# Kernel optimization log

Hardware: AMD Instinct MI355X
Metric: run time of the kernel (lower is better)

## Reference

```python
import jax, jax.numpy as jnp
import numpy as np

VOCAB = 32000
EMB = 300
DEC_UNITS = 512
UNITS = 2 * DEC_UNITS        # GRU units = 1024
ENC_DIM = 1024               # encoder output feature dim
B, S = 256, 128
IN_DIM = ENC_DIM + EMB       # GRU input: [context ; embedding] = 1324


def setup_inputs() -> dict:
    key = jax.random.key(0)
    ks = jax.random.split(key, 16)
    sc = 0.02
    return {
        "x": jax.random.randint(ks[0], (B, 1), 0, VOCAB),
        "state": jax.random.normal(ks[1], (B, UNITS), jnp.float32),
        "encoder_output": jax.random.normal(ks[2], (B, S, ENC_DIM), jnp.float32),
        "emb": jax.random.normal(ks[3], (VOCAB, EMB), jnp.float32) * sc,
        "W1": jax.random.normal(ks[4], (ENC_DIM, DEC_UNITS), jnp.float32) * sc,
        "b1": jnp.zeros((DEC_UNITS,), jnp.float32),
        "W2": jax.random.normal(ks[5], (UNITS, DEC_UNITS), jnp.float32) * sc,
        "b2": jnp.zeros((DEC_UNITS,), jnp.float32),
        "V": jax.random.normal(ks[6], (DEC_UNITS, 1), jnp.float32) * sc,
        "bV": jnp.zeros((1,), jnp.float32),
        "gru_k": jax.random.normal(ks[7], (IN_DIM, 3 * UNITS), jnp.float32) * sc,
        "gru_rk": jax.random.normal(ks[8], (UNITS, 3 * UNITS), jnp.float32) * sc,
        "gru_b": jnp.zeros((2, 3 * UNITS), jnp.float32),  # [input_bias, recurrent_bias] (reset_after=True)
        "fc_W": jax.random.normal(ks[9], (UNITS, VOCAB), jnp.float32) * sc,
        "fc_b": jnp.zeros((VOCAB,), jnp.float32),
    }


def reference(x, state, encoder_output, emb, W1, b1, W2, b2, V, bV,
              gru_k, gru_rk, gru_b, fc_W, fc_b):
    # --- Bahdanau attention (query = state, values = encoder_output) ---
    # score: [B, S, 1]
    q = state @ W2 + b2                                    # [B, U_att]
    score = jnp.tanh(encoder_output @ W1 + b1 + q[:, None, :]) @ V + bV
    attn = jax.nn.softmax(score, axis=1)                   # [B, S, 1]
    context = jnp.sum(attn * encoder_output, axis=1)       # [B, ENC_DIM]

    # --- embed token and concat with context (seq len 1) ---
    x_emb = emb[x[:, 0]]                                   # [B, EMB]
    xi = jnp.concatenate([context, x_emb], axis=-1)        # [B, IN_DIM]

    # --- single GRU step (Keras GRU, reset_after=True, inference: no dropout) ---
    mx = xi @ gru_k + gru_b[0]                             # [B, 3U]
    mh = state @ gru_rk + gru_b[1]                         # [B, 3U]
    xz, xr, xh = jnp.split(mx, 3, axis=-1)
    hz, hr, hh_rec = jnp.split(mh, 3, axis=-1)
    z = jax.nn.sigmoid(xz + hz)
    r = jax.nn.sigmoid(xr + hr)
    hh = jnp.tanh(xh + r * hh_rec)
    h = z * state + (1.0 - z) * hh                         # [B, UNITS]

    # --- softmax projection over vocab ---
    probs = jax.nn.softmax(h @ fc_W + fc_b, axis=-1)       # [B, VOCAB]
    return probs, h, attn
```

## Files before the change

### kernel.cpp

```cpp
#include <hip/hip_runtime.h>
#include <math.h>

#define B_    256
#define S_    128
#define ENCD  1024
#define DECU  512
#define UNITS 1024
#define VOCAB 32000
#define EMB_  300
#define INDIM 1324
#define KPADX 1344
#define G3    3072

typedef __bf16 bf16x8 __attribute__((ext_vector_type(8)));
typedef __bf16 bf16x4 __attribute__((ext_vector_type(4)));
typedef __bf16 bf16x2 __attribute__((ext_vector_type(2)));
typedef float  f32x4  __attribute__((ext_vector_type(4)));

#define MFMA16(a, b, c) __builtin_amdgcn_mfma_f32_16x16x32_bf16((a), (b), (c), 0, 0, 0)

__device__ __forceinline__ int swz(int row, int e) { return row * 64 + (e ^ ((row & 7) << 3)); }

__device__ __forceinline__ void gl_lds16(const void* g, void* l) {
  __builtin_amdgcn_global_load_lds((const __attribute__((address_space(1))) void*)g,
                                   (__attribute__((address_space(3))) void*)l, 16, 0, 0);
}

__device__ __forceinline__ float fast_tanh(float x) {
  x = fminf(fmaxf(x, -15.f), 15.f);
  float e = __expf(2.f * x);
  return (e - 1.f) / (e + 1.f);
}

__global__ __launch_bounds__(256) void k_prep(const float* __restrict__ enc,
                                              __bf16* __restrict__ enc_bf,
                                              const float* __restrict__ state,
                                              __bf16* __restrict__ state_bf) {
  int bid = blockIdx.x;
  if (bid < 4096) {
    for (int g = bid * 256 + threadIdx.x; g < (B_ * S_ * ENCD) / 8; g += 4096 * 256) {
      const float* p = enc + (size_t)g * 8;
      float4 f0 = *(const float4*)p;
      float4 f1 = *(const float4*)(p + 4);
      bf16x8 o = {(__bf16)f0.x, (__bf16)f0.y, (__bf16)f0.z, (__bf16)f0.w,
                  (__bf16)f1.x, (__bf16)f1.y, (__bf16)f1.z, (__bf16)f1.w};
      *(bf16x8*)(enc_bf + (size_t)g * 8) = o;
    }
  } else {
    int i4 = (bid - 4096) * 256 + threadIdx.x;
    float4 f = *(const float4*)(state + (size_t)i4 * 4);
    bf16x4 o = {(__bf16)f.x, (__bf16)f.y, (__bf16)f.z, (__bf16)f.w};
    *(bf16x4*)(state_bf + (size_t)i4 * 4) = o;
  }
}

__global__ __launch_bounds__(1024) void k_w1t(const float* __restrict__ W1,
                                              __bf16* __restrict__ W1t) {
  int n = blockIdx.x;
  int k = threadIdx.x;
  W1t[(size_t)n * 1024 + k] = (__bf16)W1[(size_t)k * 512 + n];
}

template <int BM>
__global__ __launch_bounds__(512) void k_gemm2(const __bf16* __restrict__ A, int ldaK,
                                               const float* __restrict__ B,
                                               const float* __restrict__ bias,
                                               float* __restrict__ C, int K, int N) {
  constexpr int WR = (BM == 64) ? 2 : 4;
  constexpr int WN = 8 / WR;
  constexpr int MI = BM / (WR * 16);
  constexpr int NI = 64 / (WN * 16);
  __shared__ __align__(16) __bf16 As[2][BM * 64];
  __shared__ __align__(16) __bf16 Bs[2][64 * 64];
  int tid = threadIdx.x, lane = tid & 63, w = tid >> 6;
  int wr = w / WN, wn = w % WN;
  int m0 = blockIdx.x * BM, n0 = blockIdx.y * 64;
  int lrow = lane & 15, lk = (lane >> 4) * 8;
  int r0 = wr * MI * 16, c0 = wn * NI * 16;
  f32x4 acc[MI][NI] = {};

  constexpr int ACH = BM / 64;
  constexpr int TPR = 8 / ACH;
  bf16x8 pfa[ACH];
  float pfb[8];
  int am = tid / TPR, aks = (tid % TPR) * (ACH * 8);
  const __bf16* arow = A + (size_t)(m0 + am) * ldaK + aks;
  int bn = tid & 63, bks = (tid >> 6) * 8;
  int nk = (K + 63) >> 6;

#pragma unroll
  for (int c = 0; c < ACH; ++c) pfa[c] = *(const bf16x8*)(arow + c * 8);
#pragma unroll
  for (int i = 0; i < 8; ++i) { int k = bks + i; pfb[i] = (k < K) ? B[(size_t)k * N + n0 + bn] : 0.f; }
#pragma unroll
  for (int c = 0; c < ACH; ++c) *(bf16x8*)&As[0][swz(am, aks + c * 8)] = pfa[c];
  {
    __bf16 tb[8];
#pragma unroll
    for (int i = 0; i < 8; ++i) tb[i] = (__bf16)pfb[i];
    *(bf16x8*)&Bs[0][swz(bn, bks)] = *(bf16x8*)&tb[0];
  }
  __syncthreads();

  int cur = 0;
  for (int it = 0; it < nk; ++it) {
    bool more = (it + 1 < nk);
    if (more) {
      int k0 = (it + 1) * 64;
#pragma unroll
      for (int c = 0; c < ACH; ++c) pfa[c] = *(const bf16x8*)(arow + k0 + c * 8);
#pragma unroll
      for (int i = 0; i < 8; ++i) { int k = k0 + bks + i; pfb[i] = (k < K) ? B[(size_t)k * N + n0 + bn] : 0.f; }
    }
    const __bf16* Ac = As[cur];
    const __bf16* Bc = Bs[cur];
#pragma unroll
    for (int kk = 0; kk < 64; kk += 32) {
      bf16x8 av[MI], bv[NI];
#pragma unroll
      for (int mi = 0; mi < MI; ++mi) { int r = r0 + mi * 16 + lrow; av[mi] = *(const bf16x8*)&Ac[swz(r, kk + lk)]; }
#pragma unroll
      for (int ni = 0; ni < NI; ++ni) { int r = c0 + ni * 16 + lrow; bv[ni] = *(const bf16x8*)&Bc[swz(r, kk + lk)]; }
#pragma unroll
      for (int mi = 0; mi < MI; ++mi)
#pragma unroll
        for (int ni = 0; ni < NI; ++ni) acc[mi][ni] = MFMA16(av[mi], bv[ni], acc[mi][ni]);
    }
    if (more) {
#pragma unroll
      for (int c = 0; c < ACH; ++c) *(bf16x8*)&As[cur ^ 1][swz(am, aks + c * 8)] = pfa[c];
      __bf16 tb[8];
#pragma unroll
      for (int i = 0; i < 8; ++i) tb[i] = (__bf16)pfb[i];
      *(bf16x8*)&Bs[cur ^ 1][swz(bn, bks)] = *(bf16x8*)&tb[0];
      __syncthreads();
      cur ^= 1;
    }
  }
#pragma unroll
  for (int mi = 0; mi < MI; ++mi)
#pragma unroll
    for (int ni = 0; ni < NI; ++ni) {
      int colg = n0 + c0 + ni * 16 + lrow;
      float bvv = bias[colg];
#pragma unroll
      for (int reg = 0; reg < 4; ++reg) {
        int rowg = m0 + r0 + mi * 16 + (lane >> 4) * 4 + reg;
        C[(size_t)rowg * N + colg] = acc[mi][ni][reg] + bvv;
      }
    }
}

__global__ __launch_bounds__(512) void k_gemm2d(const __bf16* __restrict__ A, int ldaK,
                                                const float* __restrict__ B1,
                                                const float* __restrict__ bias1,
                                                float* __restrict__ C1, int N1,
                                                const float* __restrict__ B2,
                                                const float* __restrict__ bias2,
                                                float* __restrict__ C2, int N2,
                                                int K) {
  constexpr int BM = 64, MI = 2, NI = 1;
  __shared__ __align__(16) __bf16 As[2][BM * 64];
  __shared__ __align__(16) __bf16 Bs[2][64 * 64];
  int tid = threadIdx.x, lane = tid & 63, w = tid >> 6;
  int wr = w >> 2, wn = w & 3;
  int m0 = blockIdx.x * BM;
  int n0 = blockIdx.y * 64;
  const float* B; const float* bias; float* C; int N;
  if (n0 < N1) { B = B1; bias = bias1; C = C1; N = N1; }
  else         { B = B2; bias = bias2; C = C2; N = N2; n0 -= N1; }
  int lrow = lane & 15, lk = (lane >> 4) * 8;
  int r0 = wr * MI * 16, c0 = wn * NI * 16;
  f32x4 acc[MI][NI] = {};

  bf16x8 pfa;
  float pfb[8];
  int am = tid >> 3, aks = (tid & 7) * 8;
  const __bf16* arow = A + (size_t)(m0 + am) * ldaK + aks;
  int bn = tid & 63, bks = (tid >> 6) * 8;
  int nk = (K + 63) >> 6;

  pfa = *(const bf16x8*)(arow);
#pragma unroll
  for (int i = 0; i < 8; ++i) { int k = bks + i; pfb[i] = (k < K) ? B[(size_t)k * N + n0 + bn] : 0.f; }
  *(bf16x8*)&As[0][swz(am, aks)] = pfa;
  {
    __bf16 tb[8];
#pragma unroll
    for (int i = 0; i < 8; ++i) tb[i] = (__bf16)pfb[i];
    *(bf16x8*)&Bs[0][swz(bn, bks)] = *(bf16x8*)&tb[0];
  }
  __syncthreads();

  int cur = 0;
  for (int it = 0; it < nk; ++it) {
    bool more = (it + 1 < nk);
    if (more) {
      int k0 = (it + 1) * 64;
      pfa = *(const bf16x8*)(arow + k0);
#pragma unroll
      for (int i = 0; i < 8; ++i) { int k = k0 + bks + i; pfb[i] = (k < K) ? B[(size_t)k * N + n0 + bn] : 0.f; }
    }
    const __bf16* Ac = As[cur];
    const __bf16* Bc = Bs[cur];
#pragma unroll
    for (int kk = 0; kk < 64; kk += 32) {
      bf16x8 av[MI], bv[NI];
#pragma unroll
      for (int mi = 0; mi < MI; ++mi) { int r = r0 + mi * 16 + lrow; av[mi] = *(const bf16x8*)&Ac[swz(r, kk + lk)]; }
#pragma unroll
      for (int ni = 0; ni < NI; ++ni) { int r = c0 + ni * 16 + lrow; bv[ni] = *(const bf16x8*)&Bc[swz(r, kk + lk)]; }
#pragma unroll
      for (int mi = 0; mi < MI; ++mi)
#pragma unroll
        for (int ni = 0; ni < NI; ++ni) acc[mi][ni] = MFMA16(av[mi], bv[ni], acc[mi][ni]);
    }
    if (more) {
      *(bf16x8*)&As[cur ^ 1][swz(am, aks)] = pfa;
      __bf16 tb[8];
#pragma unroll
      for (int i = 0; i < 8; ++i) tb[i] = (__bf16)pfb[i];
      *(bf16x8*)&Bs[cur ^ 1][swz(bn, bks)] = *(bf16x8*)&tb[0];
      __syncthreads();
      cur ^= 1;
    }
  }
#pragma unroll
  for (int mi = 0; mi < MI; ++mi)
#pragma unroll
    for (int ni = 0; ni < NI; ++ni) {
      int colg = n0 + c0 + ni * 16 + lrow;
      float bvv = bias[colg];
#pragma unroll
      for (int reg = 0; reg < 4; ++reg) {
        int rowg = m0 + r0 + mi * 16 + (lane >> 4) * 4 + reg;
        C[(size_t)rowg * N + colg] = acc[mi][ni][reg] + bvv;
      }
    }
}

__global__ __launch_bounds__(512) void k_score8(const __bf16* __restrict__ enc_bf,
                                                const __bf16* __restrict__ W1t,
                                                const float* __restrict__ b1,
                                                const float* __restrict__ q,
                                                const float* __restrict__ V,
                                                float* __restrict__ sc_part) {
  __shared__ __align__(16) __bf16 As[3][128 * 64];
  __shared__ __align__(16) __bf16 Bs[3][128 * 64];
  __shared__ float red[2][128];
  int b = blockIdx.x, by = blockIdx.y;
  int m0 = b * 128, n0 = by * 128;
  int tid = threadIdx.x, lane = tid & 63, w = tid >> 6;
  int wr = w >> 1, wn = w & 1;
  int lrow = lane & 15, lk = (lane >> 4) * 8;
  int r0 = wr * 32, c0 = wn * 64;
  f32x4 acc[2][4] = {};

  float vj[4], b1j[4], qv[4];
#pragma unroll
  for (int ni = 0; ni < 4; ++ni) {
    int j = n0 + c0 + ni * 16 + lrow;
    vj[ni] = V[j]; b1j[ni] = b1[j]; qv[ni] = q[(size_t)b * DECU + j];
  }
  int srow = lane >> 3;
  int sslot = (lane & 7) ^ (srow & 7);
  const __bf16* asrc[2];
  const __bf16* bsrc[2];
  int ch0 = w * 2;
#pragma unroll
  for (int c = 0; c < 2; ++c) {
    int row = (ch0 + c) * 8 + srow;
    asrc[c] = enc_bf + (size_t)(m0 + row) * 1024 + sslot * 8;
    bsrc[c] = W1t + (size_t)(n0 + row) * 1024 + sslot * 8;
  }
  asm volatile("s_waitcnt vmcnt(0)" ::: "memory");

#pragma unroll
  for (int t = 0; t < 2; ++t) {
    int k0 = t * 64;
#pragma unroll
    for (int c = 0; c < 2; ++c) {
      gl_lds16(asrc[c] + k0, &As[t][(ch0 + c) * 512]);
      gl_lds16(bsrc[c] + k0, &Bs[t][(ch0 + c) * 512]);
    }
  }
  asm volatile("s_waitcnt vmcnt(4)" ::: "memory");
  __builtin_amdgcn_s_barrier();

#pragma unroll
  for (int it = 0; it < 16; ++it) {
    if (it + 2 < 16) {
      int k0 = (it + 2) * 64, bi = (it + 2) % 3;
#pragma unroll
      for (int c = 0; c < 2; ++c) {
        gl_lds16(asrc[c] + k0, &As[bi][(ch0 + c) * 512]);
        gl_lds16(bsrc[c] + k0, &Bs[bi][(ch0 + c) * 512]);
      }
    }
    const __bf16* Ac = As[it % 3];
    const __bf16* Bc = Bs[it % 3];
#pragma unroll
    for (int kk = 0; kk < 64; kk += 32) {
      bf16x8 av[2], bv[4];
#pragma unroll
      for (int mi = 0; mi < 2; ++mi) { int r = r0 + mi * 16 + lrow; av[mi] = *(const bf16x8*)&Ac[swz(r, kk + lk)]; }
#pragma unroll
      for (int ni = 0; ni < 4; ++ni) { int r = c0 + ni * 16 + lrow; bv[ni] = *(const bf16x8*)&Bc[swz(r, kk + lk)]; }
#pragma unroll
      for (int mi = 0; mi < 2; ++mi)
#pragma unroll
        for (int ni = 0; ni < 4; ++ni) acc[mi][ni] = MFMA16(av[mi], bv[ni], acc[mi][ni]);
    }
    if (it < 15) {
      if (it < 14) asm volatile("s_waitcnt vmcnt(4)" ::: "memory");
      else         asm volatile("s_waitcnt vmcnt(0)" ::: "memory");
      __builtin_amdgcn_s_barrier();
    }
  }
  float psum[2][4] = {};
#pragma unroll
  for (int mi = 0; mi < 2; ++mi)
#pragma unroll
    for (int ni = 0; ni < 4; ++ni) {
#pragma unroll
      for (int reg = 0; reg < 4; ++reg)
        psum[mi][reg] += vj[ni] * fast_tanh(acc[mi][ni][reg] + b1j[ni] + qv[ni]);
    }
#pragma unroll
  for (int off = 1; off < 16; off <<= 1)
#pragma unroll
    for (int mi = 0; mi < 2; ++mi)
#pragma unroll
      for (int reg = 0; reg < 4; ++reg)
        psum[mi][reg] += __shfl_xor(psum[mi][reg], off);
  __syncthreads();
  if (lrow == 0) {
#pragma unroll
    for (int mi = 0; mi < 2; ++mi)
#pragma unroll
      for (int reg = 0; reg < 4; ++reg)
        red[wn][r0 + mi * 16 + (lane >> 4) * 4 + reg] = psum[mi][reg];
  }
  __syncthreads();
  if (tid < 128)
    sc_part[((size_t)b * 128 + tid) * 4 + by] = red[0][tid] + red[1][tid];
}

__global__ __launch_bounds__(256) void k_ctx4(const float* __restrict__ sc_part,
                                              const float* __restrict__ bV,
                                              const __bf16* __restrict__ enc_bf,
                                              const int* __restrict__ x,
                                              const float* __restrict__ emb,
                                              float* __restrict__ attn_out,
                                              __bf16* __restrict__ xi_bf) {
  int b = blockIdx.x, chunk = blockIdx.y, t = threadIdx.x;
  int lane = t & 63, w = t >> 6;
  __shared__ float a_s[S_];
  __shared__ float part[4][128];
  if (t < S_) {
    float4 p = *(const float4*)&sc_part[((size_t)b * 128 + t) * 4];
    a_s[t] = bV[0] + p.x + p.y + p.z + p.w;
  }
  __syncthreads();
  float mx = -INFINITY;
  for (int s = 0; s < S_; ++s) mx = fmaxf(mx, a_s[s]);
  float sum = 0.f;
  for (int s = 0; s < S_; ++s) sum += __expf(a_s[s] - mx);
  float inv = 1.f / sum;
  __syncthreads();
  if (t < S_) {
    float av = __expf(a_s[t] - mx) * inv;
    a_s[t] = av;
    if (chunk == 0) attn_out[(size_t)b * S_ + t] = av;
  }
  __syncthreads();
  int c0 = chunk * 128;
  float a0 = 0.f, a1 = 0.f;
  const __bf16* eb = enc_bf + ((size_t)b * S_ + w * 32) * ENCD + c0 + lane * 2;
#pragma unroll 8
  for (int s = 0; s < 32; ++s) {
    bf16x2 e = *(const bf16x2*)(eb + (size_t)s * ENCD);
    float av = a_s[w * 32 + s];
    a0 = fmaf(av, (float)e[0], a0);
    a1 = fmaf(av, (float)e[1], a1);
  }
  part[w][lane * 2 + 0] = a0;
  part[w][lane * 2 + 1] = a1;
  __syncthreads();
  if (t < 128) {
    float v = part[0][t] + part[1][t] + part[2][t] + part[3][t];
    xi_bf[(size_t)b * KPADX + c0 + t] = (__bf16)v;
  }
  if (chunk == 0) {
    int xb = x[b];
    if (t < 75) {
      float4 f = *(const float4*)&emb[(size_t)xb * EMB_ + t * 4];
      bf16x4 o4 = {(__bf16)f.x, (__bf16)f.y, (__bf16)f.z, (__bf16)f.w};
      *(bf16x4*)&xi_bf[(size_t)b * KPADX + ENCD + t * 4] = o4;
    } else if (t < 80) {
      bf16x4 z = {(__bf16)0.f, (__bf16)0.f, (__bf16)0.f, (__bf16)0.f};
      *(bf16x4*)&xi_bf[(size_t)b * KPADX + INDIM + (t - 75) * 4] = z;
    }
  }
}

__global__ __launch_bounds__(256) void k_gates(const float* __restrict__ mx,
                                               const float* __restrict__ mh,
                                               const float* __restrict__ state,
                                               float* __restrict__ h_out,
                                               __bf16* __restrict__ h_bf) {
  int idx = blockIdx.x * 256 + threadIdx.x;
  int b = idx >> 10, j = idx & 1023;
  const float* mxr = mx + (size_t)b * G3;
  const float* mhr = mh + (size_t)b * G3;
  float z = 1.f / (1.f + __expf(-(mxr[j] + mhr[j])));
  float r = 1.f / (1.f + __expf(-(mxr[UNITS + j] + mhr[UNITS + j])));
  float hh = tanhf(mxr[2 * UNITS + j] + r * mhr[2 * UNITS + j]);
  float st = state[idx];
  float h = z * st + (1.f - z) * hh;
  h_out[idx] = h;
  h_bf[idx] = (__bf16)h;
}

__global__ __launch_bounds__(1024) void k_softmax(float* __restrict__ logits) {
  int b = blockIdx.x, t = threadIdx.x;
  int lane = t & 63, w = t >> 6;
  float4* row4 = (float4*)(logits + (size_t)b * VOCAB);
  __shared__ float redm[16];
  __shared__ float reds[16];
  float4 v[8];
  float m = -INFINITY;
#pragma unroll
  for (int i = 0; i < 8; ++i) {
    int i4 = i * 1024 + t;
    if (i4 < 8000) {
      v[i] = row4[i4];
      m = fmaxf(m, fmaxf(fmaxf(v[i].x, v[i].y), fmaxf(v[i].z, v[i].w)));
    } else {
      v[i] = make_float4(-INFINITY, -INFINITY, -INFINITY, -INFINITY);
    }
  }
#pragma unroll
  for (int o = 32; o >= 1; o >>= 1) m = fmaxf(m, __shfl_xor(m, o));
  if (lane == 0) redm[w] = m;
  __syncthreads();
  float m2 = -INFINITY;
#pragma unroll
  for (int i = 0; i < 16; ++i) m2 = fmaxf(m2, redm[i]);
  float s = 0.f;
#pragma unroll
  for (int i = 0; i < 8; ++i) {
    v[i].x = __expf(v[i].x - m2);
    v[i].y = __expf(v[i].y - m2);
    v[i].z = __expf(v[i].z - m2);
    v[i].w = __expf(v[i].w - m2);
    s += v[i].x + v[i].y + v[i].z + v[i].w;
  }
#pragma unroll
  for (int o = 32; o >= 1; o >>= 1) s += __shfl_xor(s, o);
  if (lane == 0) reds[w] = s;
  __syncthreads();
  float s2 = 0.f;
#pragma unroll
  for (int i = 0; i < 16; ++i) s2 += reds[i];
  float inv = 1.f / s2;
#pragma unroll
  for (int i = 0; i < 8; ++i) {
    int i4 = i * 1024 + t;
    if (i4 < 8000)
      row4[i4] = make_float4(v[i].x * inv, v[i].y * inv, v[i].z * inv, v[i].w * inv);
  }
}

extern "C" void kernel_launch(void* const* d_in, const int* in_sizes, int n_in,
                              void* d_out, int out_size, void* d_ws, size_t ws_size,
                              hipStream_t stream) {
  const int*   x     = (const int*)d_in[0];
  const float* state = (const float*)d_in[1];
  const float* enc   = (const float*)d_in[2];
  const float* emb   = (const float*)d_in[3];
  const float* W1    = (const float*)d_in[4];
  const float* b1    = (const float*)d_in[5];
  const float* W2    = (const float*)d_in[6];
  const float* b2    = (const float*)d_in[7];
  const float* V     = (const float*)d_in[8];
  const float* bV    = (const float*)d_in[9];
  const float* gru_k = (const float*)d_in[10];
  const float* gru_rk= (const float*)d_in[11];
  const float* gru_b = (const float*)d_in[12];
  const float* fc_W  = (const float*)d_in[13];
  const float* fc_b  = (const float*)d_in[14];

  float* out   = (float*)d_out;
  float* probs = out;
  float* h_out = out + (size_t)B_ * VOCAB;
  float* attn  = h_out + (size_t)B_ * UNITS;

  char* wsb = (char*)d_ws;
  const size_t ENC_BF_BYTES = (size_t)B_ * S_ * ENCD * 2;
  __bf16* enc_bf  = (__bf16*)wsb;
  __bf16* W1t     = (__bf16*)(wsb + ENC_BF_BYTES);
  __bf16* state_bf= (__bf16*)(wsb + ENC_BF_BYTES + 1048576);
  __bf16* xi_bf   = (__bf16*)(wsb + ENC_BF_BYTES + 1572864);
  __bf16* h_bf    = (__bf16*)(wsb + ENC_BF_BYTES + 2260992);
  float*  q       = (float*)(wsb + ENC_BF_BYTES + 2785280);
  float*  sc_part = (float*)(wsb + ENC_BF_BYTES + 3309568);
  float*  mx      = (float*)(wsb + ENC_BF_BYTES + 3833856);
  float*  mh      = (float*)(wsb + ENC_BF_BYTES + 6979584);

  k_prep<<<4352, 256, 0, stream>>>(enc, enc_bf, state, state_bf);
  k_w1t<<<512, 1024, 0, stream>>>(W1, W1t);
  k_gemm2d<<<dim3(4, 56), 512, 0, stream>>>(state_bf, UNITS,
                                            gru_rk, gru_b + G3, mh, G3,
                                            W2, b2, q, DECU, UNITS);
  k_score8<<<dim3(B_, 4), 512, 0, stream>>>(enc_bf, W1t, b1, q, V, sc_part);
  k_ctx4<<<dim3(B_, 8), 256, 0, stream>>>(sc_part, bV, enc_bf, x, emb, attn, xi_bf);
  k_gemm2<64><<<dim3(4, 48), 512, 0, stream>>>(xi_bf, KPADX, gru_k, gru_b, mx, INDIM, G3);
  k_gates<<<(B_ * UNITS) / 256, 256, 0, stream>>>(mx, mh, state, h_out, h_bf);
  k_gemm2<256><<<dim3(1, VOCAB / 64), 512, 0, stream>>>(h_bf, UNITS, fc_W, fc_b, probs, UNITS, VOCAB);
  k_softmax<<<B_, 1024, 0, stream>>>(probs);
}
```

Baseline: 231.7 us.

## Enlarge attention-score GEMM tiles to 256x256 with half-tile pipelined loads

The fused attention-score kernel now computes 256x256 output tiles per block (two batch rows by half the attention units) instead of 128x128, which doubles operand reuse from LDS and halves redundant global loads of the encoder and W1 tiles. Loads are split into four half-tiles and interleaved with four MFMA sub-phases under a double buffer, with s_setprio raised around the MFMA work. The partial-score output shrinks from four column slices to two, and the context kernel is updated to sum two partials. The grid drops to 256 blocks with 64 KB+ LDS each, so occupancy and load balance across CUs may suffer.

Result: faster. 224.2 us (-3.3%).

```diff
diff --git a/kernel.cpp b/kernel.cpp
--- a/kernel.cpp
+++ b/kernel.cpp
@@ -239,114 +239,138 @@
     }
 }
 
-__global__ __launch_bounds__(512) void k_score8(const __bf16* __restrict__ enc_bf,
+__global__ __launch_bounds__(512) void k_score9(const __bf16* __restrict__ enc_bf,
                                                 const __bf16* __restrict__ W1t,
                                                 const float* __restrict__ b1,
                                                 const float* __restrict__ q,
                                                 const float* __restrict__ V,
                                                 float* __restrict__ sc_part) {
-  __shared__ __align__(16) __bf16 As[3][128 * 64];
-  __shared__ __align__(16) __bf16 Bs[3][128 * 64];
-  __shared__ float red[2][128];
-  int b = blockIdx.x, by = blockIdx.y;
-  int m0 = b * 128, n0 = by * 128;
-  int tid = threadIdx.x, lane = tid & 63, w = tid >> 6;
-  int wr = w >> 1, wn = w & 1;
+  __shared__ __align__(16) __bf16 Ah[2][2][8192];
+  __shared__ __align__(16) __bf16 Bh[2][2][8192];
+  __shared__ float red[4][256];
+  int tid = threadIdx.x, lane = tid & 63, wv = tid >> 6;
+  int wr = wv >> 2, wc = wv & 3;
   int lrow = lane & 15, lk = (lane >> 4) * 8;
-  int r0 = wr * 32, c0 = wn * 64;
-  f32x4 acc[2][4] = {};
-
-  float vj[4], b1j[4], qv[4];
-#pragma unroll
-  for (int ni = 0; ni < 4; ++ni) {
-    int j = n0 + c0 + ni * 16 + lrow;
-    vj[ni] = V[j]; b1j[ni] = b1[j]; qv[ni] = q[(size_t)b * DECU + j];
-  }
+  int m0 = blockIdx.x * 256, by = blockIdx.y, n0 = by * 256;
+
+  f32x4 acc[4][4][2] = {};
+
+  float Vv[2][2], B1v[2][2], Qv[2][2][2];
+#pragma unroll
+  for (int qc = 0; qc < 2; ++qc)
+#pragma unroll
+    for (int j = 0; j < 2; ++j) {
+      int c = n0 + qc * 128 + wc * 32 + j * 16 + lrow;
+      Vv[qc][j] = V[c];
+      B1v[qc][j] = b1[c];
+#pragma unroll
+      for (int qr = 0; qr < 2; ++qr)
+        Qv[qr][qc][j] = q[(size_t)(blockIdx.x * 2 + qr) * DECU + c];
+    }
+  asm volatile("s_waitcnt vmcnt(0)" ::: "memory");
+
   int srow = lane >> 3;
   int sslot = (lane & 7) ^ (srow & 7);
-  const __bf16* asrc[2];
-  const __bf16* bsrc[2];
-  int ch0 = w * 2;
-#pragma unroll
-  for (int c = 0; c < 2; ++c) {
-    int row = (ch0 + c) * 8 + srow;
-    asrc[c] = enc_bf + (size_t)(m0 + row) * 1024 + sslot * 8;
-    bsrc[c] = W1t + (size_t)(n0 + row) * 1024 + sslot * 8;
-  }
-  asm volatile("s_waitcnt vmcnt(0)" ::: "memory");
-
-#pragma unroll
-  for (int t = 0; t < 2; ++t) {
-    int k0 = t * 64;
-#pragma unroll
-    for (int c = 0; c < 2; ++c) {
-      gl_lds16(asrc[c] + k0, &As[t][(ch0 + c) * 512]);
-      gl_lds16(bsrc[c] + k0, &Bs[t][(ch0 + c) * 512]);
-    }
-  }
-  asm volatile("s_waitcnt vmcnt(4)" ::: "memory");
-  __builtin_amdgcn_s_barrier();
-
-#pragma unroll
-  for (int it = 0; it < 16; ++it) {
-    if (it + 2 < 16) {
-      int k0 = (it + 2) * 64, bi = (it + 2) % 3;
-#pragma unroll
-      for (int c = 0; c < 2; ++c) {
-        gl_lds16(asrc[c] + k0, &As[bi][(ch0 + c) * 512]);
-        gl_lds16(bsrc[c] + k0, &Bs[bi][(ch0 + c) * 512]);
-      }
-    }
-    const __bf16* Ac = As[it % 3];
-    const __bf16* Bc = Bs[it % 3];
-#pragma unroll
-    for (int kk = 0; kk < 64; kk += 32) {
-      bf16x8 av[2], bv[4];
-#pragma unroll
-      for (int mi = 0; mi < 2; ++mi) { int r = r0 + mi * 16 + lrow; av[mi] = *(const bf16x8*)&Ac[swz(r, kk + lk)]; }
-#pragma unroll
-      for (int ni = 0; ni < 4; ++ni) { int r = c0 + ni * 16 + lrow; bv[ni] = *(const bf16x8*)&Bc[swz(r, kk + lk)]; }
-#pragma unroll
-      for (int mi = 0; mi < 2; ++mi)
-#pragma unroll
-        for (int ni = 0; ni < 4; ++ni) acc[mi][ni] = MFMA16(av[mi], bv[ni], acc[mi][ni]);
-    }
-    if (it < 15) {
-      if (it < 14) asm volatile("s_waitcnt vmcnt(4)" ::: "memory");
-      else         asm volatile("s_waitcnt vmcnt(0)" ::: "memory");
-      __builtin_amdgcn_s_barrier();
-    }
-  }
-  float psum[2][4] = {};
-#pragma unroll
-  for (int mi = 0; mi < 2; ++mi)
-#pragma unroll
-    for (int ni = 0; ni < 4; ++ni) {
-#pragma unroll
-      for (int reg = 0; reg < 4; ++reg)
-        psum[mi][reg] += vj[ni] * fast_tanh(acc[mi][ni][reg] + b1j[ni] + qv[ni]);
-    }
+  const __bf16* aS = enc_bf + (size_t)(m0 + wv * 16 + srow) * 1024 + sslot * 8;
+  const __bf16* bS = W1t + (size_t)(n0 + wv * 16 + srow) * 1024 + sslot * 8;
+
+#define ST_A(HF, DB, KO) do { \
+    gl_lds16(aS + (size_t)(HF) * 131072 + (KO), &Ah[DB][HF][wv * 1024]); \
+    gl_lds16(aS + (size_t)(HF) * 131072 + 8192 + (KO), &Ah[DB][HF][wv * 1024 + 512]); } while (0)
+#define ST_B(HF, DB, KO) do { \
+    gl_lds16(bS + (size_t)(HF) * 131072 + (KO), &Bh[DB][HF][wv * 1024]); \
+    gl_lds16(bS + (size_t)(HF) * 131072 + 8192 + (KO), &Bh[DB][HF][wv * 1024 + 512]); } while (0)
+
+#define WORK(P, QR, QC) do { \
+    const __bf16* Ab = &Ah[rd][QR][0]; \
+    const __bf16* Bb = &Bh[rd][QC][0]; \
+    __builtin_amdgcn_s_setprio(1); \
+    _Pragma("unroll") \
+    for (int kk = 0; kk < 64; kk += 32) { \
+      bf16x8 av[4], bv[2]; \
+      _Pragma("unroll") \
+      for (int i = 0; i < 4; ++i) av[i] = *(const bf16x8*)&Ab[swz(wr * 64 + i * 16 + lrow, kk + lk)]; \
+      _Pragma("unroll") \
+      for (int j = 0; j < 2; ++j) bv[j] = *(const bf16x8*)&Bb[swz(wc * 32 + j * 16 + lrow, kk + lk)]; \
+      _Pragma("unroll") \
+      for (int i = 0; i < 4; ++i) \
+        _Pragma("unroll") \
+        for (int j = 0; j < 2; ++j) acc[P][i][j] = MFMA16(av[i], bv[j], acc[P][i][j]); \
+    } \
+    __builtin_amdgcn_s_setprio(0); } while (0)
+
+  ST_A(0, 0, 0);
+  ST_B(0, 0, 0);
+  ST_A(1, 0, 0);
+  ST_B(1, 0, 0);
+
+  for (int t = 0; t < 16; ++t) {
+    int rd = t & 1, wd = rd ^ 1;
+    size_t ko = (size_t)(t + 1) * 64;
+    bool more = (t < 15);
+    asm volatile("s_waitcnt vmcnt(4)" ::: "memory");
+    __builtin_amdgcn_s_barrier();
+    if (more) ST_A(0, wd, ko);
+    WORK(0, 0, 0);
+    asm volatile("s_waitcnt vmcnt(4)" ::: "memory");
+    __builtin_amdgcn_s_barrier();
+    if (more) ST_B(0, wd, ko);
+    WORK(1, 1, 0);
+    asm volatile("s_waitcnt vmcnt(4)" ::: "memory");
+    __builtin_amdgcn_s_barrier();
+    if (more) ST_A(1, wd, ko);
+    WORK(2, 1, 1);
+    __builtin_amdgcn_s_barrier();
+    if (more) ST_B(1, wd, ko);
+    WORK(3, 0, 1);
+  }
+#undef ST_A
+#undef ST_B
+#undef WORK
+
+  float psum[2][4][4] = {};
+  {
+    constexpr int QRv[4] = {0, 1, 1, 0};
+    constexpr int QCv[4] = {0, 0, 1, 1};
+#pragma unroll
+    for (int p = 0; p < 4; ++p) {
+      int qr = QRv[p], qc = QCv[p];
+#pragma unroll
+      for (int i = 0; i < 4; ++i)
+#pragma unroll
+        for (int j = 0; j < 2; ++j)
+#pragma unroll
+          for (int reg = 0; reg < 4; ++reg)
+            psum[qr][i][reg] += Vv[qc][j] * fast_tanh(acc[p][i][j][reg] + B1v[qc][j] + Qv[qr][qc][j]);
+    }
+  }
 #pragma unroll
   for (int off = 1; off < 16; off <<= 1)
 #pragma unroll
-    for (int mi = 0; mi < 2; ++mi)
-#pragma unroll
-      for (int reg = 0; reg < 4; ++reg)
-        psum[mi][reg] += __shfl_xor(psum[mi][reg], off);
+    for (int qr = 0; qr < 2; ++qr)
+#pragma unroll
+      for (int i = 0; i < 4; ++i)
+#pragma unroll
+        for (int reg = 0; reg < 4; ++reg)
+          psum[qr][i][reg] += __shfl_xor(psum[qr][i][reg], off);
   __syncthreads();
   if (lrow == 0) {
 #pragma unroll
-    for (int mi = 0; mi < 2; ++mi)
-#pragma unroll
-      for (int reg = 0; reg < 4; ++reg)
-        red[wn][r0 + mi * 16 + (lane >> 4) * 4 + reg] = psum[mi][reg];
-  }
-  __syncthreads();
-  if (tid < 128)
-    sc_part[((size_t)b * 128 + tid) * 4 + by] = red[0][tid] + red[1][tid];
-}
-
-__global__ __launch_bounds__(256) void k_ctx4(const float* __restrict__ sc_part,
+    for (int qr = 0; qr < 2; ++qr)
+#pragma unroll
+      for (int i = 0; i < 4; ++i)
+#pragma unroll
+        for (int reg = 0; reg < 4; ++reg)
+          red[wc][qr * 128 + wr * 64 + i * 16 + (lane >> 4) * 4 + reg] = psum[qr][i][reg];
+  }
+  __syncthreads();
+  if (tid < 256) {
+    float s = red[0][tid] + red[1][tid] + red[2][tid] + red[3][tid];
+    sc_part[(size_t)(m0 + tid) * 2 + by] = s;
+  }
+}
+
+__global__ __launch_bounds__(256) void k_ctx5(const float* __restrict__ sc_part,
                                               const float* __restrict__ bV,
                                               const __bf16* __restrict__ enc_bf,
                                               const int* __restrict__ x,
@@ -358,8 +382,8 @@
   __shared__ float a_s[S_];
   __shared__ float part[4][128];
   if (t < S_) {
-    float4 p = *(const float4*)&sc_part[((size_t)b * 128 + t) * 4];
-    a_s[t] = bV[0] + p.x + p.y + p.z + p.w;
+    float2 p = *(const float2*)&sc_part[((size_t)b * 128 + t) * 2];
+    a_s[t] = bV[0] + p.x + p.y;
   }
   __syncthreads();
   float mx = -INFINITY;
@@ -513,8 +537,8 @@
   k_gemm2d<<<dim3(4, 56), 512, 0, stream>>>(state_bf, UNITS,
                                             gru_rk, gru_b + G3, mh, G3,
                                             W2, b2, q, DECU, UNITS);
-  k_score8<<<dim3(B_, 4), 512, 0, stream>>>(enc_bf, W1t, b1, q, V, sc_part);
-  k_ctx4<<<dim3(B_, 8), 256, 0, stream>>>(sc_part, bV, enc_bf, x, emb, attn, xi_bf);
+  k_score9<<<dim3(128, 2), 512, 0, stream>>>(enc_bf, W1t, b1, q, V, sc_part);
+  k_ctx5<<<dim3(B_, 8), 256, 0, stream>>>(sc_part, bV, enc_bf, x, emb, attn, xi_bf);
   k_gemm2<64><<<dim3(4, 48), 512, 0, stream>>>(xi_bf, KPADX, gru_k, gru_b, mx, INDIM, G3);
   k_gates<<<(B_ * UNITS) / 256, 256, 0, stream>>>(mx, mh, state, h_out, h_bf);
   k_gemm2<256><<<dim3(1, VOCAB / 64), 512, 0, stream>>>(h_bf, UNITS, fc_W, fc_b, probs, UNITS, VOCAB);
```
